# Optimization experiments

Measured on AMD Instinct MI355X. Metric: run time of the kernel, lower is better.

## Reference

```python
import jax, jax.numpy as jnp
import numpy as np

EPS = 1e-5

def _bn(x, gamma, beta):
    # BatchNorm1d forward (batch statistics, biased variance) over node dim
    mu = x.mean(axis=0)
    var = x.var(axis=0)
    return gamma * (x - mu) * jax.lax.rsqrt(var + EPS) + beta

def _gcn_conv(x, W, b, src, dst, n):
    # PyG GCNConv: h = x @ W; symmetric norm with self-loops; scatter-add to dst
    h = x @ W                                   # [N, out]
    ones = jnp.ones(src.shape, dtype=h.dtype)
    deg = jax.ops.segment_sum(ones, dst, num_segments=n) + 1.0  # +1 self-loop
    dinv = jax.lax.rsqrt(deg)                   # deg >= 1 always
    norm = dinv[src] * dinv[dst]                # [E]
    agg = jax.ops.segment_sum(h[src] * norm[:, None], dst, num_segments=n)
    agg = agg + h * (dinv * dinv)[:, None]      # self-loop contribution
    return agg + b

def setup_inputs() -> dict:
    key = jax.random.key(0)
    ks = jax.random.split(key, 10)
    N, E = 100000, 1600000
    Din, Dh, Dout = 256, 128, 128
    e_prev = jax.random.normal(ks[0], (N, Din), dtype=jnp.float32)
    edge_index = jax.random.randint(ks[1], (2, E), 0, N, dtype=jnp.int64)
    proj_W = jax.random.normal(ks[2], (Din, Din), dtype=jnp.float32) * 0.02
    proj_b = jnp.zeros((Din,), dtype=jnp.float32)
    W1 = jax.random.normal(ks[3], (Din, Dh), dtype=jnp.float32) * 0.05
    b1 = jnp.zeros((Dh,), dtype=jnp.float32)
    gamma1 = jnp.ones((Dh,), dtype=jnp.float32)
    beta1 = jnp.zeros((Dh,), dtype=jnp.float32)
    W2 = jax.random.normal(ks[4], (Dh, Dout), dtype=jnp.float32) * 0.05
    b2 = jnp.zeros((Dout,), dtype=jnp.float32)
    gamma2 = jnp.ones((Dout,), dtype=jnp.float32)
    beta2 = jnp.zeros((Dout,), dtype=jnp.float32)
    return {"e_prev": e_prev, "edge_index": edge_index,
            "proj_W": proj_W, "proj_b": proj_b,
            "W1": W1, "b1": b1, "gamma1": gamma1, "beta1": beta1,
            "W2": W2, "b2": b2, "gamma2": gamma2, "beta2": beta2}

def reference(e_prev, edge_index, proj_W, proj_b, W1, b1, gamma1, beta1, W2, b2, gamma2, beta2):
    n = e_prev.shape[0]
    src, dst = edge_index[0], edge_index[1]
    # input_projection (input_dim != hidden_dim branch)
    x = e_prev @ proj_W + proj_b
    x = _gcn_conv(x, W1, b1, src, dst, n)
    x = _bn(x, gamma1, beta1)
    x = jax.nn.relu(x)
    # dropout(0.2) is identity in eval mode
    x = _gcn_conv(x, W2, b2, src, dst, n)
    x = _bn(x, gamma2, beta2)
    return x
```

## Files before the change

kernel.cpp:

```cpp
#include <hip/hip_runtime.h>
#include <hip/hip_bf16.h>
#include <math.h>

#define BN_EPS 1e-5f
#define CAP 6144
#define MAXB 512

typedef __attribute__((ext_vector_type(8))) short short8;
typedef __attribute__((ext_vector_type(4))) float floatx4;

__device__ inline float4 ntload4(const float* p) {
    floatx4 v = __builtin_nontemporal_load((const floatx4*)p);
    return make_float4(v.x, v.y, v.z, v.w);
}

__global__ __launch_bounds__(128) void prep_kernel(
    const float* __restrict__ PW, const float* __restrict__ W1,
    const float* __restrict__ pb, const float* __restrict__ W2,
    __hip_bfloat16* __restrict__ Wf1, __hip_bfloat16* __restrict__ Wf2,
    float* __restrict__ bc, int* __restrict__ bcursor, int nb)
{
    int bid = blockIdx.x;
    int tid = threadIdx.x;
    if (bid < 256) {
        int k = bid, c = tid;
        float acc = 0.f;
        for (int kk = 0; kk < 256; ++kk) acc = fmaf(PW[k * 256 + kk], W1[kk * 128 + c], acc);
        int kc = k >> 5, r5 = k & 31, qq = r5 >> 3, j = r5 & 7;
        int ct = c >> 4, l16 = c & 15;
        int lane = qq * 16 + l16;
        Wf1[(((kc * 8 + ct) * 64) + lane) * 8 + j] = __float2bfloat16(acc);
    } else if (bid == 256) {
        int c = tid;
        float acc = 0.f;
        for (int k = 0; k < 256; ++k) acc = fmaf(pb[k], W1[k * 128 + c], acc);
        bc[c] = acc;
    } else if (bid < 385) {
        int t = (bid - 257) * 128 + tid;
        int j    = t & 7;
        int lane = (t >> 3) & 63;
        int ct   = (t >> 9) & 7;
        int kc   = t >> 12;
        int k = kc * 32 + ((lane >> 4) & 3) * 8 + j;
        int c = ct * 16 + (lane & 15);
        Wf2[t] = __float2bfloat16(W2[k * 128 + c]);
    } else {
        int i = (bid - 385) * 128 + tid;
        if (i < nb) bcursor[i] = i * CAP;
    }
}

__global__ __launch_bounds__(256) void bucket_kernel(
    const int* __restrict__ src, const int* __restrict__ dst,
    int* __restrict__ bcursor, unsigned* __restrict__ buck, int E, int nb)
{
    __shared__ int h[MAXB], resv[MAXB], cur[MAXB];
    for (int t = threadIdx.x; t < nb; t += 256) { h[t] = 0; cur[t] = 0; }
    __syncthreads();
    int per = (E + gridDim.x - 1) / gridDim.x;
    int e0 = blockIdx.x * per;
    int e1 = min(e0 + per, E);
    for (int e = e0 + threadIdx.x; e < e1; e += 256) {
        int d = __builtin_nontemporal_load(&dst[e]);
        atomicAdd(&h[d >> 8], 1);
    }
    __syncthreads();
    for (int t = threadIdx.x; t < nb; t += 256) {
        int c = h[t];
        if (c > 0) resv[t] = atomicAdd(&bcursor[t], c);
    }
    __syncthreads();
    for (int e = e0 + threadIdx.x; e < e1; e += 256) {
        int d = __builtin_nontemporal_load(&dst[e]);
        int s = __builtin_nontemporal_load(&src[e]);
        int b = d >> 8;
        int pos = resv[b] + atomicAdd(&cur[b], 1);
        buck[pos] = ((unsigned)(d & 255) << 17) | (unsigned)s;
    }
}

__global__ __launch_bounds__(256) void csr_kernel(
    const unsigned* __restrict__ buck, const int* __restrict__ bcursor,
    int* __restrict__ cnt, int* __restrict__ rowptr, float* __restrict__ dinv,
    int* __restrict__ ssrc, int N)
{
    __shared__ int h[256], sc[256], lcur[256], redu[256];
    int b = blockIdx.x;
    int t = threadIdx.x;
    int part = 0;
    for (int i = t; i < b; i += 256) part += bcursor[i] - i * CAP;
    redu[t] = part;
    h[t] = 0;
    __syncthreads();
    for (int off = 128; off > 0; off >>= 1) {
        if (t < off) redu[t] += redu[t + off];
        __syncthreads();
    }
    int cb = redu[0];

    int base = b * CAP;
    int nB = bcursor[b] - base;
    for (int i = t; i < nB; i += 256) {
        unsigned v = buck[base + i];
        atomicAdd(&h[v >> 17], 1);
    }
    __syncthreads();
    int myc = h[t];
    sc[t] = myc;
    __syncthreads();
    for (int off = 1; off < 256; off <<= 1) {
        int x = (t >= off) ? sc[t - off] : 0;
        __syncthreads();
        sc[t] += x;
        __syncthreads();
    }
    int ex = sc[t] - myc;
    lcur[t] = ex;
    int node = b * 256 + t;
    if (node < N) {
        cnt[node]    = myc;
        rowptr[node] = cb + ex;
        dinv[node]   = rsqrtf((float)myc + 1.0f);
    }
    __syncthreads();
    for (int i = t; i < nB; i += 256) {
        unsigned v = buck[base + i];
        int dloc = v >> 17;
        int pos = cb + atomicAdd(&lcur[dloc], 1);
        ssrc[pos] = (int)(v & 0x1FFFFu);
    }
}

__device__ inline short8 cvt8(float4 a, float4 b) {
    __hip_bfloat162 p0 = __float22bfloat162_rn(make_float2(a.x, a.y));
    __hip_bfloat162 p1 = __float22bfloat162_rn(make_float2(a.z, a.w));
    __hip_bfloat162 p2 = __float22bfloat162_rn(make_float2(b.x, b.y));
    __hip_bfloat162 p3 = __float22bfloat162_rn(make_float2(b.z, b.w));
    union { short8 s; __hip_bfloat162 h[4]; } u;
    u.h[0] = p0; u.h[1] = p1; u.h[2] = p2; u.h[3] = p3;
    return u.s;
}

template <int K, bool BN>
__global__ __launch_bounds__(256) void mfma_gemm(
    const float* __restrict__ X, const short* __restrict__ Wf,
    const float* __restrict__ bias, const float* __restrict__ dinv,
    const float* __restrict__ scale, const float* __restrict__ shift,
    __hip_bfloat16* __restrict__ Hs, int N)
{
    const int wave = threadIdx.x >> 6;
    const int lane = threadIdx.x & 63;
    const int l16  = lane & 15;
    const int q    = lane >> 4;
    const int r0   = blockIdx.x * 128 + wave * 32;

    const int ra0 = min(r0 + l16, N - 1);
    const int ra1 = min(r0 + 16 + l16, N - 1);
    const float* pA0 = X + (size_t)ra0 * K + q * 8;
    const float* pA1 = X + (size_t)ra1 * K + q * 8;
    const short8* WF = (const short8*)Wf;

    floatx4 acc[2][8];
#pragma unroll
    for (int rt = 0; rt < 2; ++rt)
#pragma unroll
        for (int ct = 0; ct < 8; ++ct) { acc[rt][ct][0] = 0.f; acc[rt][ct][1] = 0.f; acc[rt][ct][2] = 0.f; acc[rt][ct][3] = 0.f; }

#pragma unroll
    for (int kc = 0; kc < K / 32; ++kc) {
        short8 b[8];
#pragma unroll
        for (int ct = 0; ct < 8; ++ct) b[ct] = WF[(kc * 8 + ct) * 64 + lane];

        float4 x00 = ntload4(pA0 + kc * 32);
        float4 x01 = ntload4(pA0 + kc * 32 + 4);
        float4 x10 = ntload4(pA1 + kc * 32);
        float4 x11 = ntload4(pA1 + kc * 32 + 4);
        if (BN) {
            float4 sc0 = *(const float4*)(scale + kc * 32 + q * 8);
            float4 sc1 = *(const float4*)(scale + kc * 32 + q * 8 + 4);
            float4 sh0 = *(const float4*)(shift + kc * 32 + q * 8);
            float4 sh1 = *(const float4*)(shift + kc * 32 + q * 8 + 4);
            x00.x = fmaxf(fmaf(x00.x, sc0.x, sh0.x), 0.f);
            x00.y = fmaxf(fmaf(x00.y, sc0.y, sh0.y), 0.f);
            x00.z = fmaxf(fmaf(x00.z, sc0.z, sh0.z), 0.f);
            x00.w = fmaxf(fmaf(x00.w, sc0.w, sh0.w), 0.f);
            x01.x = fmaxf(fmaf(x01.x, sc1.x, sh1.x), 0.f);
            x01.y = fmaxf(fmaf(x01.y, sc1.y, sh1.y), 0.f);
            x01.z = fmaxf(fmaf(x01.z, sc1.z, sh1.z), 0.f);
            x01.w = fmaxf(fmaf(x01.w, sc1.w, sh1.w), 0.f);
            x10.x = fmaxf(fmaf(x10.x, sc0.x, sh0.x), 0.f);
            x10.y = fmaxf(fmaf(x10.y, sc0.y, sh0.y), 0.f);
            x10.z = fmaxf(fmaf(x10.z, sc0.z, sh0.z), 0.f);
            x10.w = fmaxf(fmaf(x10.w, sc0.w, sh0.w), 0.f);
            x11.x = fmaxf(fmaf(x11.x, sc1.x, sh1.x), 0.f);
            x11.y = fmaxf(fmaf(x11.y, sc1.y, sh1.y), 0.f);
            x11.z = fmaxf(fmaf(x11.z, sc1.z, sh1.z), 0.f);
            x11.w = fmaxf(fmaf(x11.w, sc1.w, sh1.w), 0.f);
        }
        short8 a0 = cvt8(x00, x01);
        short8 a1 = cvt8(x10, x11);
#pragma unroll
        for (int ct = 0; ct < 8; ++ct) {
            acc[0][ct] = __builtin_amdgcn_mfma_f32_16x16x32_bf16(a0, b[ct], acc[0][ct], 0, 0, 0);
            acc[1][ct] = __builtin_amdgcn_mfma_f32_16x16x32_bf16(a1, b[ct], acc[1][ct], 0, 0, 0);
        }
    }

    float bb[8];
#pragma unroll
    for (int ct = 0; ct < 8; ++ct) bb[ct] = bias ? bias[ct * 16 + l16] : 0.f;

#pragma unroll
    for (int rt = 0; rt < 2; ++rt) {
        int rbase = r0 + rt * 16 + q * 4;
        float dv[4];
#pragma unroll
        for (int i = 0; i < 4; ++i) dv[i] = dinv[min(rbase + i, N - 1)];
#pragma unroll
        for (int ct = 0; ct < 8; ++ct) {
#pragma unroll
            for (int i = 0; i < 4; ++i) {
                int row = rbase + i;
                if (row < N)
                    Hs[(size_t)row * 128 + ct * 16 + l16] =
                        __float2bfloat16((acc[rt][ct][i] + bb[ct]) * dv[i]);
            }
        }
    }
}

__device__ inline void accrow(uint4 u, float* a) {
    a[0] += __uint_as_float(u.x << 16);
    a[1] += __uint_as_float(u.x & 0xffff0000u);
    a[2] += __uint_as_float(u.y << 16);
    a[3] += __uint_as_float(u.y & 0xffff0000u);
    a[4] += __uint_as_float(u.z << 16);
    a[5] += __uint_as_float(u.z & 0xffff0000u);
    a[6] += __uint_as_float(u.w << 16);
    a[7] += __uint_as_float(u.w & 0xffff0000u);
}

__global__ __launch_bounds__(256) void agg_gather_kernel(
    const uint4* __restrict__ Hq, const int* __restrict__ rowptr,
    const int* __restrict__ cnt, const int* __restrict__ ssrc,
    const float* __restrict__ dinv, const float* __restrict__ bias,
    float* __restrict__ Out, int N)
{
    int node = blockIdx.x * 4 + (threadIdx.x >> 6);
    if (node >= N) return;
    int lane = threadIdx.x & 63;
    int q    = lane >> 4;
    int l16  = lane & 15;

    float a0[8] = {0,0,0,0,0,0,0,0};
    float a1[8] = {0,0,0,0,0,0,0,0};
    float a2[8] = {0,0,0,0,0,0,0,0};
    float a3[8] = {0,0,0,0,0,0,0,0};

    if (q == 0) accrow(Hq[(size_t)node * 16 + l16], a0);

    int start = rowptr[node];
    int num   = cnt[node];
    int j = 0;
    for (; j + 16 <= num; j += 16) {
        int e = start + j + q;
        int s0 = ssrc[e];
        int s1 = ssrc[e + 4];
        int s2 = ssrc[e + 8];
        int s3 = ssrc[e + 12];
        uint4 u0 = Hq[(size_t)s0 * 16 + l16];
        uint4 u1 = Hq[(size_t)s1 * 16 + l16];
        uint4 u2 = Hq[(size_t)s2 * 16 + l16];
        uint4 u3 = Hq[(size_t)s3 * 16 + l16];
        accrow(u0, a0);
        accrow(u1, a1);
        accrow(u2, a2);
        accrow(u3, a3);
    }
    for (; j + 4 <= num; j += 4) {
        int s = ssrc[start + j + q];
        accrow(Hq[(size_t)s * 16 + l16], a0);
    }
    int rem = num - j;
    if (q < rem) {
        int s = ssrc[start + j + q];
        accrow(Hq[(size_t)s * 16 + l16], a1);
    }

#pragma unroll
    for (int i = 0; i < 8; ++i) {
        float v = a0[i] + a1[i] + a2[i] + a3[i];
        v += __shfl_xor(v, 16, 64);
        v += __shfl_xor(v, 32, 64);
        a0[i] = v;
    }

    if (q == 0) {
        float di = dinv[node];
        const float4* B4 = (const float4*)bias;
        float4 bb0 = B4[l16 * 2];
        float4 bb1 = B4[l16 * 2 + 1];
        float4 o0, o1;
        o0.x = fmaf(a0[0], di, bb0.x);
        o0.y = fmaf(a0[1], di, bb0.y);
        o0.z = fmaf(a0[2], di, bb0.z);
        o0.w = fmaf(a0[3], di, bb0.w);
        o1.x = fmaf(a0[4], di, bb1.x);
        o1.y = fmaf(a0[5], di, bb1.y);
        o1.z = fmaf(a0[6], di, bb1.z);
        o1.w = fmaf(a0[7], di, bb1.w);
        float4* O4 = (float4*)(Out + (size_t)node * 128 + l16 * 8);
        O4[0] = o0;
        O4[1] = o1;
    }
}

__global__ __launch_bounds__(256) void bn_stats_kernel(
    const float* __restrict__ A, float* __restrict__ partS, float* __restrict__ partQ,
    int N, int R)
{
    int col4   = threadIdx.x & 31;
    int rowoff = threadIdx.x >> 5;
    int r0 = blockIdx.x * R;
    int r1 = min(r0 + R, N);
    float4 s = make_float4(0.f, 0.f, 0.f, 0.f);
    float4 qq = make_float4(0.f, 0.f, 0.f, 0.f);
#pragma unroll 4
    for (int r = r0 + rowoff; r < r1; r += 8) {
        float4 v = *(const float4*)&A[(size_t)r * 128 + col4 * 4];
        s.x += v.x; s.y += v.y; s.z += v.z; s.w += v.w;
        qq.x = fmaf(v.x, v.x, qq.x);
        qq.y = fmaf(v.y, v.y, qq.y);
        qq.z = fmaf(v.z, v.z, qq.z);
        qq.w = fmaf(v.w, v.w, qq.w);
    }
    __shared__ float4 ls[256], lq[256];
    ls[threadIdx.x] = s;
    lq[threadIdx.x] = qq;
    __syncthreads();
    if (threadIdx.x < 32) {
        float4 ts = ls[threadIdx.x], tq = lq[threadIdx.x];
#pragma unroll
        for (int k = 1; k < 8; ++k) {
            float4 xs = ls[k * 32 + threadIdx.x];
            float4 xq = lq[k * 32 + threadIdx.x];
            ts.x += xs.x; ts.y += xs.y; ts.z += xs.z; ts.w += xs.w;
            tq.x += xq.x; tq.y += xq.y; tq.z += xq.z; tq.w += xq.w;
        }
        *(float4*)&partS[(size_t)blockIdx.x * 128 + threadIdx.x * 4] = ts;
        *(float4*)&partQ[(size_t)blockIdx.x * 128 + threadIdx.x * 4] = tq;
    }
}

__global__ void bn_final_kernel(const float* __restrict__ partS, const float* __restrict__ partQ,
                                int npart,
                                float* __restrict__ mu, float* __restrict__ rstd,
                                const float* __restrict__ gamma, const float* __restrict__ beta,
                                float* __restrict__ scale, float* __restrict__ shift, int N) {
    int c = threadIdx.x;
    if (c < 128) {
        float s = 0.f, q = 0.f;
        for (int b = 0; b < npart; ++b) {
            s += partS[(size_t)b * 128 + c];
            q += partQ[(size_t)b * 128 + c];
        }
        float m = s / (float)N;
        float v = q / (float)N - m * m;
        float rs = rsqrtf(v + BN_EPS);
        mu[c] = m;
        rstd[c] = rs;
        if (scale) {
            float sc = gamma[c] * rs;
            scale[c] = sc;
            shift[c] = fmaf(-m, sc, beta[c]);
        }
    }
}

__global__ void bn_apply_kernel(float* __restrict__ A, const float* __restrict__ gamma,
                                const float* __restrict__ beta, const float* __restrict__ mu,
                                const float* __restrict__ rstd, int N) {
    int i = blockIdx.x * blockDim.x + threadIdx.x;
    if (i >= N * 32) return;
    int c4 = i & 31;
    float4 v  = ((float4*)A)[i];
    float4 g  = ((const float4*)gamma)[c4];
    float4 b  = ((const float4*)beta)[c4];
    float4 m  = ((const float4*)mu)[c4];
    float4 rs = ((const float4*)rstd)[c4];
    v.x = fmaf(g.x * (v.x - m.x), rs.x, b.x);
    v.y = fmaf(g.y * (v.y - m.y), rs.y, b.y);
    v.z = fmaf(g.z * (v.z - m.z), rs.z, b.z);
    v.w = fmaf(g.w * (v.w - m.w), rs.w, b.w);
    ((float4*)A)[i] = v;
}

extern "C" void kernel_launch(void* const* d_in, const int* in_sizes, int n_in,
                              void* d_out, int out_size, void* d_ws, size_t ws_size,
                              hipStream_t stream) {
    const float* e_prev = (const float*)d_in[0];
    const int*   edges  = (const int*)d_in[1];
    const float* proj_W = (const float*)d_in[2];
    const float* proj_b = (const float*)d_in[3];
    const float* W1     = (const float*)d_in[4];
    const float* b1     = (const float*)d_in[5];
    const float* gamma1 = (const float*)d_in[6];
    const float* beta1  = (const float*)d_in[7];
    const float* W2     = (const float*)d_in[8];
    const float* b2     = (const float*)d_in[9];
    const float* gamma2 = (const float*)d_in[10];
    const float* beta2  = (const float*)d_in[11];
    float* out = (float*)d_out;

    const int N = in_sizes[0] / 256;
    const int E = in_sizes[1] / 2;
    const int* src = edges;
    const int* dst = edges + E;
    const int nb = (N + 255) >> 8;
    const int R = (N + 255) / 256;

    char* p = (char*)d_ws;
    const size_t NH = (size_t)N * 128;
    __hip_bfloat16* Hs = (__hip_bfloat16*)p;  p += NH * 2;
    unsigned* buck  = (unsigned*)p; p += (size_t)nb * CAP * 4;
    int* ssrc   = (int*)p;  p += (size_t)E * 4;
    int* cnt    = (int*)p;  p += (size_t)N * 4;
    int* rowptr = (int*)p;  p += (size_t)N * 4;
    float* dinv = (float*)p; p += (size_t)N * 4;
    int* bcursor = (int*)p; p += (size_t)(nb + 16) * 4;
    float* bc   = (float*)p; p += 128 * 4;
    float* stats = (float*)p; p += 1536 * 4;
    float* partS = (float*)p; p += 256 * 128 * 4;
    float* partQ = (float*)p; p += 256 * 128 * 4;
    __hip_bfloat16* Wf1 = (__hip_bfloat16*)p; p += 256 * 128 * 2;
    __hip_bfloat16* Wf2 = (__hip_bfloat16*)p; p += 128 * 128 * 2;
    float* mu1 = stats + 256, *rs1 = stats + 384;
    float* mu2 = stats + 768, *rs2 = stats + 896;
    float* scale1 = stats + 1024, *shift1 = stats + 1152;

    prep_kernel<<<389, 128, 0, stream>>>(proj_W, W1, proj_b, W2, Wf1, Wf2, bc, bcursor, nb);
    bucket_kernel<<<512, 256, 0, stream>>>(src, dst, bcursor, buck, E, nb);
    csr_kernel<<<nb, 256, 0, stream>>>(buck, bcursor, cnt, rowptr, dinv, ssrc, N);

    const int gemm_grid = (N + 127) / 128;

    mfma_gemm<256, false><<<gemm_grid, 256, 0, stream>>>(
        e_prev, (const short*)Wf1, bc, dinv, nullptr, nullptr, Hs, N);
    agg_gather_kernel<<<(N + 3) / 4, 256, 0, stream>>>(
        (const uint4*)Hs, rowptr, cnt, ssrc, dinv, b1, out, N);
    bn_stats_kernel<<<256, 256, 0, stream>>>(out, partS, partQ, N, R);
    bn_final_kernel<<<1, 128, 0, stream>>>(partS, partQ, 256, mu1, rs1,
                                           gamma1, beta1, scale1, shift1, N);

    mfma_gemm<128, true><<<gemm_grid, 256, 0, stream>>>(
        out, (const short*)Wf2, nullptr, dinv, scale1, shift1, Hs, N);
    agg_gather_kernel<<<(N + 3) / 4, 256, 0, stream>>>(
        (const uint4*)Hs, rowptr, cnt, ssrc, dinv, b2, out, N);
    bn_stats_kernel<<<256, 256, 0, stream>>>(out, partS, partQ, N, R);
    bn_final_kernel<<<1, 128, 0, stream>>>(partS, partQ, 256, mu2, rs2,
                                           nullptr, nullptr, nullptr, nullptr, N);
    bn_apply_kernel<<<(N * 32 + 255) / 256, 256, 0, stream>>>(out, gamma2, beta2, mu2, rs2, N);
}
```

Measured before the change: 609.1 us.

## Fuse BN statistics into gather via atomics and software-pipeline neighbor loads

The BatchNorm sum and sum-of-squares reduction now happens inside the aggregation kernel. Each node adds its output into one of 128 slotted partial buffers with float atomics, which removes the separate stats kernel and its extra pass over the output. The gather loop is also restructured into a two-stage software pipeline: indices for the next 16 edges are prefetched, and tail edges are handled with clamped indices and predication instead of separate remainder loops. This trades one full read of the N×128 output for 16 atomics per node, adds contention on the partial slots, and makes the summation order nondeterministic.

Result: slower. 2.094 ms (+243.8%).

```diff
diff --git a/kernel.cpp b/kernel.cpp
--- a/kernel.cpp
+++ b/kernel.cpp
@@ -18,7 +18,8 @@
     const float* __restrict__ PW, const float* __restrict__ W1,
     const float* __restrict__ pb, const float* __restrict__ W2,
     __hip_bfloat16* __restrict__ Wf1, __hip_bfloat16* __restrict__ Wf2,
-    float* __restrict__ bc, int* __restrict__ bcursor, int nb)
+    float* __restrict__ bc, int* __restrict__ bcursor,
+    float* __restrict__ pstat, int nb)
 {
     int bid = blockIdx.x;
     int tid = threadIdx.x;
@@ -44,9 +45,12 @@
         int k = kc * 32 + ((lane >> 4) & 3) * 8 + j;
         int c = ct * 16 + (lane & 15);
         Wf2[t] = __float2bfloat16(W2[k * 128 + c]);
-    } else {
+    } else if (bid < 389) {
         int i = (bid - 385) * 128 + tid;
         if (i < nb) bcursor[i] = i * CAP;
+    } else {
+        int i = (bid - 389) * 128 + tid;
+        pstat[i] = 0.f;
     }
 }
 
@@ -245,13 +249,14 @@
     const uint4* __restrict__ Hq, const int* __restrict__ rowptr,
     const int* __restrict__ cnt, const int* __restrict__ ssrc,
     const float* __restrict__ dinv, const float* __restrict__ bias,
-    float* __restrict__ Out, int N)
+    float* __restrict__ Out, float* __restrict__ partS, float* __restrict__ partQ,
+    int N)
 {
     int node = blockIdx.x * 4 + (threadIdx.x >> 6);
     if (node >= N) return;
-    int lane = threadIdx.x & 63;
-    int q    = lane >> 4;
-    int l16  = lane & 15;
+    const int lane = threadIdx.x & 63;
+    const int q    = lane >> 4;
+    const int l16  = lane & 15;
 
     float a0[8] = {0,0,0,0,0,0,0,0};
     float a1[8] = {0,0,0,0,0,0,0,0};
@@ -260,32 +265,43 @@
 
     if (q == 0) accrow(Hq[(size_t)node * 16 + l16], a0);
 
-    int start = rowptr[node];
-    int num   = cnt[node];
-    int j = 0;
-    for (; j + 16 <= num; j += 16) {
-        int e = start + j + q;
-        int s0 = ssrc[e];
-        int s1 = ssrc[e + 4];
-        int s2 = ssrc[e + 8];
-        int s3 = ssrc[e + 12];
+    const int start = rowptr[node];
+    const int num   = cnt[node];
+
+    if (num > 0) {
+        const int last = start + num - 1;
+        const int e0 = start + q;
+        int s0 = ssrc[min(e0,      last)];
+        int s1 = ssrc[min(e0 + 4,  last)];
+        int s2 = ssrc[min(e0 + 8,  last)];
+        int s3 = ssrc[min(e0 + 12, last)];
         uint4 u0 = Hq[(size_t)s0 * 16 + l16];
         uint4 u1 = Hq[(size_t)s1 * 16 + l16];
         uint4 u2 = Hq[(size_t)s2 * 16 + l16];
         uint4 u3 = Hq[(size_t)s3 * 16 + l16];
-        accrow(u0, a0);
-        accrow(u1, a1);
-        accrow(u2, a2);
-        accrow(u3, a3);
-    }
-    for (; j + 4 <= num; j += 4) {
-        int s = ssrc[start + j + q];
-        accrow(Hq[(size_t)s * 16 + l16], a0);
-    }
-    int rem = num - j;
-    if (q < rem) {
-        int s = ssrc[start + j + q];
-        accrow(Hq[(size_t)s * 16 + l16], a1);
+        int t0 = ssrc[min(e0 + 16, last)];
+        int t1 = ssrc[min(e0 + 20, last)];
+        int t2 = ssrc[min(e0 + 24, last)];
+        int t3 = ssrc[min(e0 + 28, last)];
+
+        const int nst = (num + 15) >> 4;
+        for (int st = 0; st < nst; ++st) {
+            uint4 v0 = Hq[(size_t)t0 * 16 + l16];
+            uint4 v1 = Hq[(size_t)t1 * 16 + l16];
+            uint4 v2 = Hq[(size_t)t2 * 16 + l16];
+            uint4 v3 = Hq[(size_t)t3 * 16 + l16];
+            int en = e0 + (st + 2) * 16;
+            t0 = ssrc[min(en,      last)];
+            t1 = ssrc[min(en + 4,  last)];
+            t2 = ssrc[min(en + 8,  last)];
+            t3 = ssrc[min(en + 12, last)];
+            int base = st * 16 + q;
+            if (base      < num) accrow(u0, a0);
+            if (base + 4  < num) accrow(u1, a1);
+            if (base + 8  < num) accrow(u2, a2);
+            if (base + 12 < num) accrow(u3, a3);
+            u0 = v0; u1 = v1; u2 = v2; u3 = v3;
+        }
     }
 
 #pragma unroll
@@ -313,43 +329,25 @@
         float4* O4 = (float4*)(Out + (size_t)node * 128 + l16 * 8);
         O4[0] = o0;
         O4[1] = o1;
-    }
-}
-
-__global__ __launch_bounds__(256) void bn_stats_kernel(
-    const float* __restrict__ A, float* __restrict__ partS, float* __restrict__ partQ,
-    int N, int R)
-{
-    int col4   = threadIdx.x & 31;
-    int rowoff = threadIdx.x >> 5;
-    int r0 = blockIdx.x * R;
-    int r1 = min(r0 + R, N);
-    float4 s = make_float4(0.f, 0.f, 0.f, 0.f);
-    float4 qq = make_float4(0.f, 0.f, 0.f, 0.f);
-#pragma unroll 4
-    for (int r = r0 + rowoff; r < r1; r += 8) {
-        float4 v = *(const float4*)&A[(size_t)r * 128 + col4 * 4];
-        s.x += v.x; s.y += v.y; s.z += v.z; s.w += v.w;
-        qq.x = fmaf(v.x, v.x, qq.x);
-        qq.y = fmaf(v.y, v.y, qq.y);
-        qq.z = fmaf(v.z, v.z, qq.z);
-        qq.w = fmaf(v.w, v.w, qq.w);
-    }
-    __shared__ float4 ls[256], lq[256];
-    ls[threadIdx.x] = s;
-    lq[threadIdx.x] = qq;
-    __syncthreads();
-    if (threadIdx.x < 32) {
-        float4 ts = ls[threadIdx.x], tq = lq[threadIdx.x];
-#pragma unroll
-        for (int k = 1; k < 8; ++k) {
-            float4 xs = ls[k * 32 + threadIdx.x];
-            float4 xq = lq[k * 32 + threadIdx.x];
-            ts.x += xs.x; ts.y += xs.y; ts.z += xs.z; ts.w += xs.w;
-            tq.x += xq.x; tq.y += xq.y; tq.z += xq.z; tq.w += xq.w;
-        }
-        *(float4*)&partS[(size_t)blockIdx.x * 128 + threadIdx.x * 4] = ts;
-        *(float4*)&partQ[(size_t)blockIdx.x * 128 + threadIdx.x * 4] = tq;
+        int sl = (blockIdx.x & 127) << 7;
+        float* ps = partS + sl + l16 * 8;
+        float* pq = partQ + sl + l16 * 8;
+        atomicAdd(&ps[0], o0.x);
+        atomicAdd(&ps[1], o0.y);
+        atomicAdd(&ps[2], o0.z);
+        atomicAdd(&ps[3], o0.w);
+        atomicAdd(&ps[4], o1.x);
+        atomicAdd(&ps[5], o1.y);
+        atomicAdd(&ps[6], o1.z);
+        atomicAdd(&ps[7], o1.w);
+        atomicAdd(&pq[0], o0.x * o0.x);
+        atomicAdd(&pq[1], o0.y * o0.y);
+        atomicAdd(&pq[2], o0.z * o0.z);
+        atomicAdd(&pq[3], o0.w * o0.w);
+        atomicAdd(&pq[4], o1.x * o1.x);
+        atomicAdd(&pq[5], o1.y * o1.y);
+        atomicAdd(&pq[6], o1.z * o1.z);
+        atomicAdd(&pq[7], o1.w * o1.w);
     }
 }
 
@@ -418,7 +416,6 @@
     const int* src = edges;
     const int* dst = edges + E;
     const int nb = (N + 255) >> 8;
-    const int R = (N + 255) / 256;
 
     char* p = (char*)d_ws;
     const size_t NH = (size_t)N * 128;
@@ -431,15 +428,16 @@
     int* bcursor = (int*)p; p += (size_t)(nb + 16) * 4;
     float* bc   = (float*)p; p += 128 * 4;
     float* stats = (float*)p; p += 1536 * 4;
-    float* partS = (float*)p; p += 256 * 128 * 4;
-    float* partQ = (float*)p; p += 256 * 128 * 4;
+    float* pstat = (float*)p; p += 65536 * 4;
     __hip_bfloat16* Wf1 = (__hip_bfloat16*)p; p += 256 * 128 * 2;
     __hip_bfloat16* Wf2 = (__hip_bfloat16*)p; p += 128 * 128 * 2;
     float* mu1 = stats + 256, *rs1 = stats + 384;
     float* mu2 = stats + 768, *rs2 = stats + 896;
     float* scale1 = stats + 1024, *shift1 = stats + 1152;
-
-    prep_kernel<<<389, 128, 0, stream>>>(proj_W, W1, proj_b, W2, Wf1, Wf2, bc, bcursor, nb);
+    float* pS1 = pstat, *pQ1 = pstat + 16384;
+    float* pS2 = pstat + 32768, *pQ2 = pstat + 49152;
+
+    prep_kernel<<<901, 128, 0, stream>>>(proj_W, W1, proj_b, W2, Wf1, Wf2, bc, bcursor, pstat, nb);
     bucket_kernel<<<512, 256, 0, stream>>>(src, dst, bcursor, buck, E, nb);
     csr_kernel<<<nb, 256, 0, stream>>>(buck, bcursor, cnt, rowptr, dinv, ssrc, N);
 
@@ -448,17 +446,15 @@
     mfma_gemm<256, false><<<gemm_grid, 256, 0, stream>>>(
         e_prev, (const short*)Wf1, bc, dinv, nullptr, nullptr, Hs, N);
     agg_gather_kernel<<<(N + 3) / 4, 256, 0, stream>>>(
-        (const uint4*)Hs, rowptr, cnt, ssrc, dinv, b1, out, N);
-    bn_stats_kernel<<<256, 256, 0, stream>>>(out, partS, partQ, N, R);
-    bn_final_kernel<<<1, 128, 0, stream>>>(partS, partQ, 256, mu1, rs1,
+        (const uint4*)Hs, rowptr, cnt, ssrc, dinv, b1, out, pS1, pQ1, N);
+    bn_final_kernel<<<1, 128, 0, stream>>>(pS1, pQ1, 128, mu1, rs1,
                                            gamma1, beta1, scale1, shift1, N);
 
     mfma_gemm<128, true><<<gemm_grid, 256, 0, stream>>>(
         out, (const short*)Wf2, nullptr, dinv, scale1, shift1, Hs, N);
     agg_gather_kernel<<<(N + 3) / 4, 256, 0, stream>>>(
-        (const uint4*)Hs, rowptr, cnt, ssrc, dinv, b2, out, N);
-    bn_stats_kernel<<<256, 256, 0, stream>>>(out, partS, partQ, N, R);
-    bn_final_kernel<<<1, 128, 0, stream>>>(partS, partQ, 256, mu2, rs2,
+        (const uint4*)Hs, rowptr, cnt, ssrc, dinv, b2, out, pS2, pQ2, N);
+    bn_final_kernel<<<1, 128, 0, stream>>>(pS2, pQ2, 128, mu2, rs2,
                                            nullptr, nullptr, nullptr, nullptr, N);
     bn_apply_kernel<<<(N * 32 + 255) / 256, 256, 0, stream>>>(out, gamma2, beta2, mu2, rs2, N);
 }
```
